# Performance work log

Hardware: AMD Instinct MI355X
Metric: run time of the kernel (lower is better)

## Reference

```python
import jax, jax.numpy as jnp
import numpy as np

B, T, C = 2, 2048, 1024
NH, NKV, HD = 16, 4, 64
VEC = 32  # ve_gate_channels


def _rope(x, cos, sin):
    d = x.shape[-1] // 2
    x1, x2 = x[..., :d], x[..., d:]
    return jnp.concatenate([x1 * cos + x2 * sin, -x1 * sin + x2 * cos], axis=-1)


def _rmsnorm(x):
    eps = jnp.finfo(x.dtype).eps
    return x * jax.lax.rsqrt(jnp.mean(x * x, axis=-1, keepdims=True) + eps)


def setup_inputs() -> dict:
    key = jax.random.key(0)
    ks = jax.random.split(key, 9)
    s = 0.02
    return {
        "x": jax.random.normal(ks[0], (B, T, C), jnp.float32),
        "ve": jax.random.normal(ks[1], (B, T, NKV * HD), jnp.float32),
        "cos": jax.random.normal(ks[2], (1, T, 1, HD // 2), jnp.float32),
        "sin": jax.random.normal(ks[3], (1, T, 1, HD // 2), jnp.float32),
        "Wq": jax.random.normal(ks[4], (C, NH * HD), jnp.float32) * s,
        "Wk": jax.random.normal(ks[5], (C, NKV * HD), jnp.float32) * s,
        "Wv": jax.random.normal(ks[6], (C, NKV * HD), jnp.float32) * s,
        "Wproj": jax.random.normal(ks[7], (C, C), jnp.float32) * s,
        "Wgate": jax.random.normal(ks[8], (VEC, NKV), jnp.float32) * s,
        "window_size": 1024,
    }


def reference(x, ve, cos, sin, Wq, Wk, Wv, Wproj, Wgate, window_size):
    Bx, Tx, Cx = x.shape
    q = (x @ Wq).reshape(Bx, Tx, NH, HD)
    k = (x @ Wk).reshape(Bx, Tx, NKV, HD)
    v = (x @ Wv).reshape(Bx, Tx, NKV, HD)

    # value-embedding gate (has_ve True for this layer)
    gate = 2.0 * jax.nn.sigmoid(x[..., :VEC] @ Wgate)  # [B,T,NKV]
    v = v + gate[..., None] * ve.reshape(Bx, Tx, NKV, HD)

    q, k = _rope(q, cos, sin), _rope(k, cos, sin)
    q, k = _rmsnorm(q), _rmsnorm(k)

    q = q.transpose(0, 2, 1, 3)  # [B,NH,T,HD]
    k = k.transpose(0, 2, 1, 3)  # [B,NKV,T,HD]
    v = v.transpose(0, 2, 1, 3)

    # GQA: each KV head serves NH//NKV consecutive q heads
    g = NH // NKV
    k = jnp.repeat(k, g, axis=1)
    v = jnp.repeat(v, g, axis=1)

    row = jnp.arange(Tx)[:, None]
    col = jnp.arange(Tx)[None, :]
    mask = (col <= row) & (col >= row - window_size)  # causal sliding window

    scores = jnp.einsum("bhqd,bhkd->bhqk", q, k) / np.sqrt(HD).astype(np.float32)
    scores = jnp.where(mask[None, None], scores, jnp.finfo(scores.dtype).min)
    attn = jax.nn.softmax(scores, axis=-1)
    y = jnp.einsum("bhqk,bhkd->bhqd", attn, v)

    y = y.transpose(0, 2, 1, 3).reshape(Bx, Tx, Cx)
    return y @ Wproj
```

## Files before the change

### kernel.cpp

```cpp
#include <hip/hip_runtime.h>

typedef __bf16 bf16x8 __attribute__((ext_vector_type(8)));
typedef __bf16 bf16x4 __attribute__((ext_vector_type(4)));
typedef float f32x4 __attribute__((ext_vector_type(4)));

__device__ inline float tof(float v) { return v; }
__device__ inline float tof(__bf16 v) { return (float)v; }

__device__ inline bf16x8 load8(const __bf16* p) { return *(const bf16x8*)p; }
__device__ inline bf16x8 load8(const float* p) {
    const float4 a = *(const float4*)p;
    const float4 b = *(const float4*)(p + 4);
    bf16x8 r;
    r[0] = (__bf16)a.x; r[1] = (__bf16)a.y; r[2] = (__bf16)a.z; r[3] = (__bf16)a.w;
    r[4] = (__bf16)b.x; r[5] = (__bf16)b.y; r[6] = (__bf16)b.z; r[7] = (__bf16)b.w;
    return r;
}

__device__ __forceinline__ void cp16(__bf16* lds, const __bf16* g) {
    __builtin_amdgcn_global_load_lds((__attribute__((address_space(1))) void*)g,
                                     (__attribute__((address_space(3))) void*)lds,
                                     16, 0, 0);
}

__global__ void sniff_kernel(const unsigned short* __restrict__ xs, int* flag) {
    int tid = threadIdx.x;
    int bad = 0;
    for (int i = tid; i < 512; i += 64) {
        unsigned int f = ((unsigned int)xs[i]) << 16;
        float v = __uint_as_float(f);
        float a = fabsf(v);
        if (!(a <= 1e4f) || (a != 0.f && a < 1e-6f)) bad++;
    }
    bad += __shfl_xor(bad, 1);  bad += __shfl_xor(bad, 2);
    bad += __shfl_xor(bad, 4);  bad += __shfl_xor(bad, 8);
    bad += __shfl_xor(bad, 16); bad += __shfl_xor(bad, 32);
    if (tid == 0) *flag = (bad > 32) ? 1 : 0;
}

template <typename T>
__device__ __forceinline__ void prep_body(
    const T* __restrict__ x, const T* __restrict__ ve,
    const T* __restrict__ cosp, const T* __restrict__ sinp,
    const T* __restrict__ Wq, const T* __restrict__ Wk,
    const T* __restrict__ Wv, const T* __restrict__ Wp, const T* __restrict__ Wg,
    __bf16* __restrict__ xb, __bf16* __restrict__ veb,
    float* __restrict__ cosf_, float* __restrict__ sinf_,
    __bf16* __restrict__ WqT, __bf16* __restrict__ WkT,
    __bf16* __restrict__ WvT, __bf16* __restrict__ WpT,
    float* __restrict__ gate, __bf16* tile)
{
    const int b = blockIdx.x, tid = threadIdx.x;

    if (b < 2624) {
        int g = b * 256 + tid;
        if (g < 524288) {
            *(bf16x8*)(xb + (size_t)g * 8) = load8(x + (size_t)g * 8);
        } else if (g < 655360) {
            int gg = g - 524288;
            *(bf16x8*)(veb + (size_t)gg * 8) = load8(ve + (size_t)gg * 8);
        } else if (g < 663552) {
            int gg = g - 655360;
            const T* s = cosp + (size_t)gg * 8; float* d = cosf_ + (size_t)gg * 8;
#pragma unroll
            for (int j = 0; j < 8; ++j) d[j] = tof(s[j]);
        } else {
            int gg = g - 663552;
            const T* s = sinp + (size_t)gg * 8; float* d = sinf_ + (size_t)gg * 8;
#pragma unroll
            for (int j = 0; j < 8; ++j) d[j] = tof(s[j]);
        }
    } else if (b < 3264) {
        int idx = b - 2624;
        const T* src; __bf16* dst; int C;
        if (idx < 256)      { src = Wq; dst = WqT; C = 1024; }
        else if (idx < 320) { src = Wk; dst = WkT; C = 256;  idx -= 256; }
        else if (idx < 384) { src = Wv; dst = WvT; C = 256;  idx -= 320; }
        else                { src = Wp; dst = WpT; C = 1024; idx -= 384; }
        const int ctiles = C >> 6;
        const int r0 = (idx / ctiles) * 64, c0 = (idx % ctiles) * 64;
#pragma unroll
        for (int i = 0; i < 2; ++i) {
            int c = tid + i * 256, ir = c >> 3, ic = (c & 7) * 8;
            *(bf16x8*)(&tile[ir * 72 + ic]) = load8(src + (size_t)(r0 + ir) * C + c0 + ic);
        }
        __syncthreads();
#pragma unroll
        for (int i = 0; i < 2; ++i) {
            int c = tid + i * 256, orr = c >> 3, okc = (c & 7) * 8;
            bf16x8 v;
#pragma unroll
            for (int j = 0; j < 8; ++j) v[j] = tile[(okc + j) * 72 + orr];
            *(bf16x8*)(dst + (size_t)(c0 + orr) * 1024 + r0 + okc) = v;
        }
    } else {
        int r = (b - 3264) * 256 + tid;
        float z[4] = {0.f, 0.f, 0.f, 0.f};
        for (int j = 0; j < 32; ++j) {
            float xv = tof(x[(size_t)r * 1024 + j]);
#pragma unroll
            for (int h = 0; h < 4; ++h) z[h] += xv * tof(Wg[j * 4 + h]);
        }
#pragma unroll
        for (int h = 0; h < 4; ++h) gate[r * 4 + h] = 2.f / (1.f + __expf(-z[h]));
    }
}

__global__ __launch_bounds__(256) void prep_kernel(
    const void* x, const void* ve, const void* cosp, const void* sinp,
    const void* Wq, const void* Wk, const void* Wv, const void* Wp, const void* Wg,
    __bf16* xb, __bf16* veb, float* cosf_, float* sinf_,
    __bf16* WqT, __bf16* WkT, __bf16* WvT, __bf16* WpT,
    float* gate, const int* __restrict__ flag)
{
    __shared__ __bf16 tile[64 * 72];
    if (*flag) {
        prep_body<float>((const float*)x, (const float*)ve, (const float*)cosp,
                         (const float*)sinp, (const float*)Wq, (const float*)Wk,
                         (const float*)Wv, (const float*)Wp, (const float*)Wg,
                         xb, veb, cosf_, sinf_, WqT, WkT, WvT, WpT, gate, tile);
    } else {
        prep_body<__bf16>((const __bf16*)x, (const __bf16*)ve, (const __bf16*)cosp,
                          (const __bf16*)sinp, (const __bf16*)Wq, (const __bf16*)Wk,
                          (const __bf16*)Wv, (const __bf16*)Wp, (const __bf16*)Wg,
                          xb, veb, cosf_, sinf_, WqT, WkT, WvT, WpT, gate, tile);
    }
}

__global__ __launch_bounds__(256) void qkv_kernel(
    const __bf16* __restrict__ xb,
    const __bf16* __restrict__ WqT, const __bf16* __restrict__ WkT,
    const __bf16* __restrict__ WvT, const __bf16* __restrict__ veb,
    const float* __restrict__ cosf_, const float* __restrict__ sinf_,
    const float* __restrict__ gate,
    __bf16* __restrict__ qo, __bf16* __restrict__ ko, __bf16* __restrict__ vTo)
{
    const int row0 = blockIdx.x * 128;
    const int cb = blockIdx.y;
    const __bf16* BT; int col0, h, mode;
    if (cb < 16)      { BT = WqT; col0 = cb * 64;        h = cb;      mode = 0; }
    else if (cb < 20) { BT = WkT; col0 = (cb - 16) * 64; h = cb - 16; mode = 1; }
    else              { BT = WvT; col0 = (cb - 20) * 64; h = cb - 20; mode = 2; }

    __shared__ __align__(16) __bf16 As[128 * 32];
    __shared__ __align__(16) __bf16 Bs[64 * 32];

    const int tid  = threadIdx.x;
    const int w    = tid >> 6;
    const int lane = tid & 63;
    const int quad = lane >> 4;
    const int l15  = lane & 15;
    const int wr   = w * 32;

    f32x4 acc[2][4];
#pragma unroll
    for (int mi = 0; mi < 2; ++mi)
#pragma unroll
        for (int nj = 0; nj < 4; ++nj) acc[mi][nj] = (f32x4){0.f, 0.f, 0.f, 0.f};

    for (int kk = 0; kk < 1024; kk += 32) {
#pragma unroll
        for (int i = 0; i < 2; ++i) {
            int c = i * 256 + (w << 6) + lane;
            int rr = c >> 2, kc = (c & 3) << 3;
            cp16(&As[c << 3], &xb[(size_t)(row0 + rr) * 1024 + kk + kc]);
        }
        {
            int c = (w << 6) + lane;
            int rr = c >> 2, kc = (c & 3) << 3;
            cp16(&Bs[c << 3], &BT[(size_t)(col0 + rr) * 1024 + kk + kc]);
        }
        __syncthreads();
        bf16x8 a[2], bfr[4];
#pragma unroll
        for (int mi = 0; mi < 2; ++mi) a[mi]  = *(const bf16x8*)(&As[(wr + mi * 16 + l15) * 32 + quad * 8]);
#pragma unroll
        for (int nj = 0; nj < 4; ++nj) bfr[nj] = *(const bf16x8*)(&Bs[(nj * 16 + l15) * 32 + quad * 8]);
#pragma unroll
        for (int mi = 0; mi < 2; ++mi)
#pragma unroll
            for (int nj = 0; nj < 4; ++nj)
                acc[mi][nj] = __builtin_amdgcn_mfma_f32_16x16x32_bf16(a[mi], bfr[nj], acc[mi][nj], 0, 0, 0);
        __syncthreads();
    }

    if (mode < 2) {
        __bf16* dst = (mode == 0) ? qo : ko;
        const int nh = (mode == 0) ? 16 : 4;
#pragma unroll
        for (int mi = 0; mi < 2; ++mi) {
#pragma unroll
            for (int r = 0; r < 4; ++r) {
                int row = row0 + wr + mi * 16 + quad * 4 + r;
                int b = row >> 11, t = row & 2047;
                float c0 = cosf_[t * 32 + l15];
                float c1 = cosf_[t * 32 + 16 + l15];
                float s0 = sinf_[t * 32 + l15];
                float s1 = sinf_[t * 32 + 16 + l15];
                float v0 =  c0 * acc[mi][0][r] + s0 * acc[mi][2][r];
                float v1 =  c1 * acc[mi][1][r] + s1 * acc[mi][3][r];
                float v2 = -s0 * acc[mi][0][r] + c0 * acc[mi][2][r];
                float v3 = -s1 * acc[mi][1][r] + c1 * acc[mi][3][r];
                float ss = v0 * v0 + v1 * v1 + v2 * v2 + v3 * v3;
                ss += __shfl_xor(ss, 1); ss += __shfl_xor(ss, 2);
                ss += __shfl_xor(ss, 4); ss += __shfl_xor(ss, 8);
                float sc = rsqrtf(ss * (1.f / 64.f) + 1.1920929e-7f);
                size_t base = (((size_t)b * nh + h) * 2048 + t) * 64;
                dst[base + 0 * 16 + l15] = (__bf16)(v0 * sc);
                dst[base + 1 * 16 + l15] = (__bf16)(v1 * sc);
                dst[base + 2 * 16 + l15] = (__bf16)(v2 * sc);
                dst[base + 3 * 16 + l15] = (__bf16)(v3 * sc);
            }
        }
    } else {
#pragma unroll
        for (int mi = 0; mi < 2; ++mi) {
            int rowb = row0 + wr + mi * 16 + quad * 4;
            int b = rowb >> 11, t0 = rowb & 2047;
#pragma unroll
            for (int nj = 0; nj < 4; ++nj) {
                int d = nj * 16 + l15;
                bf16x4 pack;
#pragma unroll
                for (int r = 0; r < 4; ++r) {
                    int row = rowb + r;
                    float g = gate[row * 4 + h];
                    float val = acc[mi][nj][r] + g * tof(veb[(size_t)row * 256 + h * 64 + d]);
                    pack[r] = (__bf16)val;
                }
                size_t a = (((size_t)b * 4 + h) * 64 + d) * 2048 + t0;
                *(bf16x4*)(&vTo[a]) = pack;
            }
        }
    }
}

__global__ __launch_bounds__(256) void attn_kernel(
    const __bf16* __restrict__ qg, const __bf16* __restrict__ kg,
    const __bf16* __restrict__ vTg, __bf16* __restrict__ yo,
    const int* __restrict__ winp)
{
    const int q0 = blockIdx.x * 128;
    const int hh = blockIdx.y, b = blockIdx.z;
    const int kvh = hh >> 2;
    const int W = winp[0];

    const int tid  = threadIdx.x;
    const int w    = tid >> 6;
    const int lane = tid & 63;
    const int quad = lane >> 4;
    const int l15  = lane & 15;

    __shared__ __align__(16) __bf16 Ks[2][64 * 64];
    __shared__ __align__(16) __bf16 Vt[2][64 * 64];
    __shared__ __align__(16) __bf16 Ps[4][32 * 72];

    bf16x8 qf[2][2];
#pragma unroll
    for (int i = 0; i < 2; ++i) {
        size_t qb = (((size_t)b * 16 + hh) * 2048 + q0 + w * 32 + i * 16 + l15) * 64;
        qf[i][0] = *(const bf16x8*)(&qg[qb + quad * 8]);
        qf[i][1] = *(const bf16x8*)(&qg[qb + 32 + quad * 8]);
    }

    f32x4 oacc[2][4];
    float lsum[2][4];
#pragma unroll
    for (int i = 0; i < 2; ++i)
#pragma unroll
        for (int n = 0; n < 4; ++n) {
            oacc[i][n] = (f32x4){0.f, 0.f, 0.f, 0.f};
            lsum[i][n] = 0.f;
        }

    const int lo = q0 - W;
    const int kt_lo = lo > 0 ? (lo >> 6) : 0;
    const int kt_hi = (q0 + 127) >> 6;
    const size_t kvbase = ((size_t)b * 4 + kvh) * 2048 * 64;

    auto stage = [&](int buf, int k0) {
#pragma unroll
        for (int i = 0; i < 2; ++i) {
            int c = i * 256 + tid;
            int rr = c >> 3;
            int jj = (c & 7) ^ (rr & 7);
            cp16(&Ks[buf][c * 8], &kg[kvbase + (size_t)(k0 + rr) * 64 + jj * 8]);
            cp16(&Vt[buf][c * 8], &vTg[kvbase + (size_t)rr * 2048 + k0 + jj * 8]);
        }
    };

    stage(0, kt_lo * 64);
    __syncthreads();

    int cur = 0;
    for (int kt = kt_lo; kt <= kt_hi; ++kt) {
        const int k0 = kt * 64;
        const bool need_mask = (k0 + 63 > q0) || (q0 + 127 - k0 > W);
        if (kt < kt_hi) stage(cur ^ 1, k0 + 64);

        f32x4 sacc[2][4];
#pragma unroll
        for (int i = 0; i < 2; ++i)
#pragma unroll
            for (int n = 0; n < 4; ++n) sacc[i][n] = (f32x4){0.f, 0.f, 0.f, 0.f};
        const __bf16* Kc = &Ks[cur][0];
#pragma unroll
        for (int n = 0; n < 4; ++n) {
            int m = n * 16 + l15;
            bf16x8 b0 = *(const bf16x8*)(&Kc[m * 64 + (quad ^ (m & 7)) * 8]);
            bf16x8 b1 = *(const bf16x8*)(&Kc[m * 64 + ((4 + quad) ^ (m & 7)) * 8]);
#pragma unroll
            for (int i = 0; i < 2; ++i) {
                sacc[i][n] = __builtin_amdgcn_mfma_f32_16x16x32_bf16(qf[i][0], b0, sacc[i][n], 0, 0, 0);
                sacc[i][n] = __builtin_amdgcn_mfma_f32_16x16x32_bf16(qf[i][1], b1, sacc[i][n], 0, 0, 0);
            }
        }

#pragma unroll
        for (int i = 0; i < 2; ++i) {
#pragma unroll
            for (int r = 0; r < 4; ++r) {
                const int row_g = q0 + w * 32 + i * 16 + quad * 4 + r;
#pragma unroll
                for (int n = 0; n < 4; ++n) {
                    float p = exp2f(fmaf(sacc[i][n][r], 0.18033688f, -11.5415603f));
                    if (need_mask) {
                        int col_g = k0 + n * 16 + l15;
                        bool ok = (col_g <= row_g) && (row_g - col_g <= W);
                        p = ok ? p : 0.f;
                    }
                    lsum[i][r] += p;
                    Ps[w][(i * 16 + quad * 4 + r) * 72 + n * 16 + l15] = (__bf16)p;
                }
            }
        }
        asm volatile("s_waitcnt lgkmcnt(0)" ::: "memory");

        const __bf16* Vc = &Vt[cur][0];
#pragma unroll
        for (int ks = 0; ks < 2; ++ks) {
            bf16x8 pfr0 = *(const bf16x8*)(&Ps[w][l15 * 72 + ks * 32 + quad * 8]);
            bf16x8 pfr1 = *(const bf16x8*)(&Ps[w][(16 + l15) * 72 + ks * 32 + quad * 8]);
#pragma unroll
            for (int n = 0; n < 4; ++n) {
                int m = n * 16 + l15;
                bf16x8 bv = *(const bf16x8*)(&Vc[m * 64 + ((ks * 4 + quad) ^ (m & 7)) * 8]);
                oacc[0][n] = __builtin_amdgcn_mfma_f32_16x16x32_bf16(pfr0, bv, oacc[0][n], 0, 0, 0);
                oacc[1][n] = __builtin_amdgcn_mfma_f32_16x16x32_bf16(pfr1, bv, oacc[1][n], 0, 0, 0);
            }
        }

        __syncthreads();
        cur ^= 1;
    }

#pragma unroll
    for (int i = 0; i < 2; ++i) {
#pragma unroll
        for (int r = 0; r < 4; ++r) {
            float l = lsum[i][r];
            l += __shfl_xor(l, 1); l += __shfl_xor(l, 2);
            l += __shfl_xor(l, 4); l += __shfl_xor(l, 8);
            float inv = 1.f / l;
            int t = q0 + w * 32 + i * 16 + quad * 4 + r;
            size_t base = ((size_t)(b * 2048 + t)) * 1024 + hh * 64;
#pragma unroll
            for (int n = 0; n < 4; ++n)
                yo[base + n * 16 + l15] = (__bf16)(oacc[i][n][r] * inv);
        }
    }
}

__global__ __launch_bounds__(256) void proj_kernel(
    const __bf16* __restrict__ y, const __bf16* __restrict__ WpT,
    void* __restrict__ outp, const int* __restrict__ flag)
{
    const int isf32 = *flag;
    const int row0 = blockIdx.x * 128;
    const int col0 = blockIdx.y * 64;
    __shared__ __align__(16) __bf16 As[128 * 32];
    __shared__ __align__(16) __bf16 Bs[64 * 32];

    const int tid  = threadIdx.x;
    const int w    = tid >> 6;
    const int lane = tid & 63;
    const int quad = lane >> 4;
    const int l15  = lane & 15;
    const int wr   = w * 32;

    f32x4 acc[2][4];
#pragma unroll
    for (int mi = 0; mi < 2; ++mi)
#pragma unroll
        for (int nj = 0; nj < 4; ++nj) acc[mi][nj] = (f32x4){0.f, 0.f, 0.f, 0.f};

    for (int kk = 0; kk < 1024; kk += 32) {
#pragma unroll
        for (int i = 0; i < 2; ++i) {
            int c = i * 256 + (w << 6) + lane;
            int rr = c >> 2, kc = (c & 3) << 3;
            cp16(&As[c << 3], &y[(size_t)(row0 + rr) * 1024 + kk + kc]);
        }
        {
            int c = (w << 6) + lane;
            int rr = c >> 2, kc = (c & 3) << 3;
            cp16(&Bs[c << 3], &WpT[(size_t)(col0 + rr) * 1024 + kk + kc]);
        }
        __syncthreads();
        bf16x8 a[2], bfr[4];
#pragma unroll
        for (int mi = 0; mi < 2; ++mi) a[mi]  = *(const bf16x8*)(&As[(wr + mi * 16 + l15) * 32 + quad * 8]);
#pragma unroll
        for (int nj = 0; nj < 4; ++nj) bfr[nj] = *(const bf16x8*)(&Bs[(nj * 16 + l15) * 32 + quad * 8]);
#pragma unroll
        for (int mi = 0; mi < 2; ++mi)
#pragma unroll
            for (int nj = 0; nj < 4; ++nj)
                acc[mi][nj] = __builtin_amdgcn_mfma_f32_16x16x32_bf16(a[mi], bfr[nj], acc[mi][nj], 0, 0, 0);
        __syncthreads();
    }

#pragma unroll
    for (int mi = 0; mi < 2; ++mi)
#pragma unroll
        for (int r = 0; r < 4; ++r) {
            int row = row0 + wr + mi * 16 + quad * 4 + r;
            if (isf32) {
                float* out = (float*)outp;
#pragma unroll
                for (int nj = 0; nj < 4; ++nj)
                    out[(size_t)row * 1024 + col0 + nj * 16 + l15] = acc[mi][nj][r];
            } else {
                __bf16* out = (__bf16*)outp;
#pragma unroll
                for (int nj = 0; nj < 4; ++nj)
                    out[(size_t)row * 1024 + col0 + nj * 16 + l15] = (__bf16)acc[mi][nj][r];
            }
        }
}

extern "C" void kernel_launch(void* const* d_in, const int* in_sizes, int n_in,
                              void* d_out, int out_size, void* d_ws, size_t ws_size,
                              hipStream_t stream) {
    const int* win = (const int*)d_in[9];

    char* p = (char*)d_ws;
    int*    flag = (int*)p;                    p += 256;
    __bf16* q_ws = (__bf16*)p;                 p += (size_t)4194304 * 2;
    __bf16* k_ws = (__bf16*)p;                 p += (size_t)1048576 * 2;
    __bf16* vT_ws= (__bf16*)p;                 p += (size_t)1048576 * 2;
    __bf16* y_ws = (__bf16*)p;                 p += (size_t)4194304 * 2;
    __bf16* xb   = (__bf16*)p;                 p += (size_t)4194304 * 2;
    __bf16* veb  = (__bf16*)p;                 p += (size_t)1048576 * 2;
    __bf16* WqT  = (__bf16*)p;                 p += (size_t)1048576 * 2;
    __bf16* WkT  = (__bf16*)p;                 p += (size_t)262144 * 2;
    __bf16* WvT  = (__bf16*)p;                 p += (size_t)262144 * 2;
    __bf16* WpT  = (__bf16*)p;                 p += (size_t)1048576 * 2;
    float*  cosf_ = (float*)p;                 p += (size_t)65536 * 4;
    float*  sinf_ = (float*)p;                 p += (size_t)65536 * 4;
    float*  gate  = (float*)p;                 p += (size_t)16384 * 4;

    sniff_kernel<<<1, 64, 0, stream>>>((const unsigned short*)d_in[0], flag);

    prep_kernel<<<3280, 256, 0, stream>>>(
        d_in[0], d_in[1], d_in[2], d_in[3], d_in[4], d_in[5], d_in[6], d_in[7],
        d_in[8], xb, veb, cosf_, sinf_, WqT, WkT, WvT, WpT, gate, flag);

    qkv_kernel<<<dim3(32, 24), 256, 0, stream>>>(xb, WqT, WkT, WvT, veb,
                                                 cosf_, sinf_, gate, q_ws, k_ws, vT_ws);

    attn_kernel<<<dim3(16, 16, 2), 256, 0, stream>>>(q_ws, k_ws, vT_ws, y_ws, win);

    proj_kernel<<<dim3(32, 16), 256, 0, stream>>>(y_ws, WpT, d_out, flag);
}
```

Before: 195.5 us.

## Fuse value-gate compute into QKV GEMM and halve attention query tile

```diff
diff --git a/kernel.cpp b/kernel.cpp
--- a/kernel.cpp
+++ b/kernel.cpp
@@ -48,11 +48,11 @@
     float* __restrict__ cosf_, float* __restrict__ sinf_,
     __bf16* __restrict__ WqT, __bf16* __restrict__ WkT,
     __bf16* __restrict__ WvT, __bf16* __restrict__ WpT,
-    float* __restrict__ gate, __bf16* tile)
+    __bf16* __restrict__ wgb, __bf16* tile)
 {
     const int b = blockIdx.x, tid = threadIdx.x;
 
-    if (b < 2624) {
+    if (b < 2625) {
         int g = b * 256 + tid;
         if (g < 524288) {
             *(bf16x8*)(xb + (size_t)g * 8) = load8(x + (size_t)g * 8);
@@ -64,14 +64,19 @@
             const T* s = cosp + (size_t)gg * 8; float* d = cosf_ + (size_t)gg * 8;
 #pragma unroll
             for (int j = 0; j < 8; ++j) d[j] = tof(s[j]);
-        } else {
+        } else if (g < 671744) {
             int gg = g - 663552;
             const T* s = sinp + (size_t)gg * 8; float* d = sinf_ + (size_t)gg * 8;
 #pragma unroll
             for (int j = 0; j < 8; ++j) d[j] = tof(s[j]);
-        }
-    } else if (b < 3264) {
-        int idx = b - 2624;
+        } else if (g < 671760) {
+            int gg = g - 671744;
+            const T* s = Wg + (size_t)gg * 8; __bf16* d = wgb + (size_t)gg * 8;
+#pragma unroll
+            for (int j = 0; j < 8; ++j) d[j] = (__bf16)tof(s[j]);
+        }
+    } else {
+        int idx = b - 2625;
         const T* src; __bf16* dst; int C;
         if (idx < 256)      { src = Wq; dst = WqT; C = 1024; }
         else if (idx < 320) { src = Wk; dst = WkT; C = 256;  idx -= 256; }
@@ -93,16 +98,6 @@
             for (int j = 0; j < 8; ++j) v[j] = tile[(okc + j) * 72 + orr];
             *(bf16x8*)(dst + (size_t)(c0 + orr) * 1024 + r0 + okc) = v;
         }
-    } else {
-        int r = (b - 3264) * 256 + tid;
-        float z[4] = {0.f, 0.f, 0.f, 0.f};
-        for (int j = 0; j < 32; ++j) {
-            float xv = tof(x[(size_t)r * 1024 + j]);
-#pragma unroll
-            for (int h = 0; h < 4; ++h) z[h] += xv * tof(Wg[j * 4 + h]);
-        }
-#pragma unroll
-        for (int h = 0; h < 4; ++h) gate[r * 4 + h] = 2.f / (1.f + __expf(-z[h]));
     }
 }
 
@@ -111,19 +106,19 @@
     const void* Wq, const void* Wk, const void* Wv, const void* Wp, const void* Wg,
     __bf16* xb, __bf16* veb, float* cosf_, float* sinf_,
     __bf16* WqT, __bf16* WkT, __bf16* WvT, __bf16* WpT,
-    float* gate, const int* __restrict__ flag)
+    __bf16* wgb, const int* __restrict__ flag)
 {
     __shared__ __bf16 tile[64 * 72];
     if (*flag) {
         prep_body<float>((const float*)x, (const float*)ve, (const float*)cosp,
                          (const float*)sinp, (const float*)Wq, (const float*)Wk,
                          (const float*)Wv, (const float*)Wp, (const float*)Wg,
-                         xb, veb, cosf_, sinf_, WqT, WkT, WvT, WpT, gate, tile);
+                         xb, veb, cosf_, sinf_, WqT, WkT, WvT, WpT, wgb, tile);
     } else {
         prep_body<__bf16>((const __bf16*)x, (const __bf16*)ve, (const __bf16*)cosp,
                           (const __bf16*)sinp, (const __bf16*)Wq, (const __bf16*)Wk,
                           (const __bf16*)Wv, (const __bf16*)Wp, (const __bf16*)Wg,
-                          xb, veb, cosf_, sinf_, WqT, WkT, WvT, WpT, gate, tile);
+                          xb, veb, cosf_, sinf_, WqT, WkT, WvT, WpT, wgb, tile);
     }
 }
 
@@ -132,7 +127,7 @@
     const __bf16* __restrict__ WqT, const __bf16* __restrict__ WkT,
     const __bf16* __restrict__ WvT, const __bf16* __restrict__ veb,
     const float* __restrict__ cosf_, const float* __restrict__ sinf_,
-    const float* __restrict__ gate,
+    const __bf16* __restrict__ wgb,
     __bf16* __restrict__ qo, __bf16* __restrict__ ko, __bf16* __restrict__ vTo)
 {
     const int row0 = blockIdx.x * 128;
@@ -158,6 +153,17 @@
 #pragma unroll
         for (int nj = 0; nj < 4; ++nj) acc[mi][nj] = (f32x4){0.f, 0.f, 0.f, 0.f};
 
+    bf16x8 wgB;
+#pragma unroll
+    for (int j = 0; j < 8; ++j) wgB[j] = (__bf16)0.f;
+    if (mode == 2 && l15 < 4) {
+#pragma unroll
+        for (int j = 0; j < 8; ++j) wgB[j] = wgb[(quad * 8 + j) * 4 + l15];
+    }
+    f32x4 zacc[2];
+    zacc[0] = (f32x4){0.f, 0.f, 0.f, 0.f};
+    zacc[1] = (f32x4){0.f, 0.f, 0.f, 0.f};
+
     for (int kk = 0; kk < 1024; kk += 32) {
 #pragma unroll
         for (int i = 0; i < 2; ++i) {
@@ -176,6 +182,10 @@
         for (int mi = 0; mi < 2; ++mi) a[mi]  = *(const bf16x8*)(&As[(wr + mi * 16 + l15) * 32 + quad * 8]);
 #pragma unroll
         for (int nj = 0; nj < 4; ++nj) bfr[nj] = *(const bf16x8*)(&Bs[(nj * 16 + l15) * 32 + quad * 8]);
+        if (mode == 2 && kk == 0) {
+            zacc[0] = __builtin_amdgcn_mfma_f32_16x16x32_bf16(a[0], wgB, zacc[0], 0, 0, 0);
+            zacc[1] = __builtin_amdgcn_mfma_f32_16x16x32_bf16(a[1], wgB, zacc[1], 0, 0, 0);
+        }
 #pragma unroll
         for (int mi = 0; mi < 2; ++mi)
 #pragma unroll
@@ -217,6 +227,12 @@
         for (int mi = 0; mi < 2; ++mi) {
             int rowb = row0 + wr + mi * 16 + quad * 4;
             int b = rowb >> 11, t0 = rowb & 2047;
+            float gg[4];
+#pragma unroll
+            for (int r = 0; r < 4; ++r) {
+                float zv = __shfl(zacc[mi][r], quad * 16 + h);
+                gg[r] = 2.f / (1.f + __expf(-zv));
+            }
 #pragma unroll
             for (int nj = 0; nj < 4; ++nj) {
                 int d = nj * 16 + l15;
@@ -224,8 +240,7 @@
 #pragma unroll
                 for (int r = 0; r < 4; ++r) {
                     int row = rowb + r;
-                    float g = gate[row * 4 + h];
-                    float val = acc[mi][nj][r] + g * tof(veb[(size_t)row * 256 + h * 64 + d]);
+                    float val = acc[mi][nj][r] + gg[r] * tof(veb[(size_t)row * 256 + h * 64 + d]);
                     pack[r] = (__bf16)val;
                 }
                 size_t a = (((size_t)b * 4 + h) * 64 + d) * 2048 + t0;
@@ -240,7 +255,7 @@
     const __bf16* __restrict__ vTg, __bf16* __restrict__ yo,
     const int* __restrict__ winp)
 {
-    const int q0 = blockIdx.x * 128;
+    const int q0 = blockIdx.x * 64;
     const int hh = blockIdx.y, b = blockIdx.z;
     const int kvh = hh >> 2;
     const int W = winp[0];
@@ -253,29 +268,20 @@
 
     __shared__ __align__(16) __bf16 Ks[2][64 * 64];
     __shared__ __align__(16) __bf16 Vt[2][64 * 64];
-    __shared__ __align__(16) __bf16 Ps[4][32 * 72];
-
-    bf16x8 qf[2][2];
-#pragma unroll
-    for (int i = 0; i < 2; ++i) {
-        size_t qb = (((size_t)b * 16 + hh) * 2048 + q0 + w * 32 + i * 16 + l15) * 64;
-        qf[i][0] = *(const bf16x8*)(&qg[qb + quad * 8]);
-        qf[i][1] = *(const bf16x8*)(&qg[qb + 32 + quad * 8]);
-    }
-
-    f32x4 oacc[2][4];
-    float lsum[2][4];
-#pragma unroll
-    for (int i = 0; i < 2; ++i)
-#pragma unroll
-        for (int n = 0; n < 4; ++n) {
-            oacc[i][n] = (f32x4){0.f, 0.f, 0.f, 0.f};
-            lsum[i][n] = 0.f;
-        }
+    __shared__ __align__(16) __bf16 Ps[4][16 * 72];
+
+    const size_t qb = (((size_t)b * 16 + hh) * 2048 + q0 + w * 16 + l15) * 64;
+    bf16x8 qf0 = *(const bf16x8*)(&qg[qb + quad * 8]);
+    bf16x8 qf1 = *(const bf16x8*)(&qg[qb + 32 + quad * 8]);
+
+    f32x4 oacc[4];
+    float lsum[4];
+#pragma unroll
+    for (int n = 0; n < 4; ++n) { oacc[n] = (f32x4){0.f, 0.f, 0.f, 0.f}; lsum[n] = 0.f; }
 
     const int lo = q0 - W;
     const int kt_lo = lo > 0 ? (lo >> 6) : 0;
-    const int kt_hi = (q0 + 127) >> 6;
+    const int kt_hi = q0 >> 6;
     const size_t kvbase = ((size_t)b * 4 + kvh) * 2048 * 64;
 
     auto stage = [&](int buf, int k0) {
@@ -295,43 +301,35 @@
     int cur = 0;
     for (int kt = kt_lo; kt <= kt_hi; ++kt) {
         const int k0 = kt * 64;
-        const bool need_mask = (k0 + 63 > q0) || (q0 + 127 - k0 > W);
+        const bool need_mask = (k0 + 63 > q0) || (q0 + 63 - k0 > W);
         if (kt < kt_hi) stage(cur ^ 1, k0 + 64);
 
-        f32x4 sacc[2][4];
-#pragma unroll
-        for (int i = 0; i < 2; ++i)
-#pragma unroll
-            for (int n = 0; n < 4; ++n) sacc[i][n] = (f32x4){0.f, 0.f, 0.f, 0.f};
+        f32x4 sacc[4];
+#pragma unroll
+        for (int n = 0; n < 4; ++n) sacc[n] = (f32x4){0.f, 0.f, 0.f, 0.f};
         const __bf16* Kc = &Ks[cur][0];
 #pragma unroll
         for (int n = 0; n < 4; ++n) {
             int m = n * 16 + l15;
             bf16x8 b0 = *(const bf16x8*)(&Kc[m * 64 + (quad ^ (m & 7)) * 8]);
             bf16x8 b1 = *(const bf16x8*)(&Kc[m * 64 + ((4 + quad) ^ (m & 7)) * 8]);
-#pragma unroll
-            for (int i = 0; i < 2; ++i) {
-                sacc[i][n] = __builtin_amdgcn_mfma_f32_16x16x32_bf16(qf[i][0], b0, sacc[i][n], 0, 0, 0);
-                sacc[i][n] = __builtin_amdgcn_mfma_f32_16x16x32_bf16(qf[i][1], b1, sacc[i][n], 0, 0, 0);
-            }
-        }
-
-#pragma unroll
-        for (int i = 0; i < 2; ++i) {
-#pragma unroll
-            for (int r = 0; r < 4; ++r) {
-                const int row_g = q0 + w * 32 + i * 16 + quad * 4 + r;
-#pragma unroll
-                for (int n = 0; n < 4; ++n) {
-                    float p = exp2f(fmaf(sacc[i][n][r], 0.18033688f, -11.5415603f));
-                    if (need_mask) {
-                        int col_g = k0 + n * 16 + l15;
-                        bool ok = (col_g <= row_g) && (row_g - col_g <= W);
-                        p = ok ? p : 0.f;
-                    }
-                    lsum[i][r] += p;
-                    Ps[w][(i * 16 + quad * 4 + r) * 72 + n * 16 + l15] = (__bf16)p;
+            sacc[n] = __builtin_amdgcn_mfma_f32_16x16x32_bf16(qf0, b0, sacc[n], 0, 0, 0);
+            sacc[n] = __builtin_amdgcn_mfma_f32_16x16x32_bf16(qf1, b1, sacc[n], 0, 0, 0);
+        }
+
+#pragma unroll
+        for (int r = 0; r < 4; ++r) {
+            const int row_g = q0 + w * 16 + quad * 4 + r;
+#pragma unroll
+            for (int n = 0; n < 4; ++n) {
+                float p = exp2f(fmaf(sacc[n][r], 0.18033688f, -11.5415603f));
+                if (need_mask) {
+                    int col_g = k0 + n * 16 + l15;
+                    bool ok = (col_g <= row_g) && (row_g - col_g <= W);
+                    p = ok ? p : 0.f;
                 }
+                lsum[r] += p;
+                Ps[w][(quad * 4 + r) * 72 + n * 16 + l15] = (__bf16)p;
             }
         }
         asm volatile("s_waitcnt lgkmcnt(0)" ::: "memory");
@@ -339,14 +337,12 @@
         const __bf16* Vc = &Vt[cur][0];
 #pragma unroll
         for (int ks = 0; ks < 2; ++ks) {
-            bf16x8 pfr0 = *(const bf16x8*)(&Ps[w][l15 * 72 + ks * 32 + quad * 8]);
-            bf16x8 pfr1 = *(const bf16x8*)(&Ps[w][(16 + l15) * 72 + ks * 32 + quad * 8]);
+            bf16x8 pfr = *(const bf16x8*)(&Ps[w][l15 * 72 + ks * 32 + quad * 8]);
 #pragma unroll
             for (int n = 0; n < 4; ++n) {
                 int m = n * 16 + l15;
                 bf16x8 bv = *(const bf16x8*)(&Vc[m * 64 + ((ks * 4 + quad) ^ (m & 7)) * 8]);
-                oacc[0][n] = __builtin_amdgcn_mfma_f32_16x16x32_bf16(pfr0, bv, oacc[0][n], 0, 0, 0);
-                oacc[1][n] = __builtin_amdgcn_mfma_f32_16x16x32_bf16(pfr1, bv, oacc[1][n], 0, 0, 0);
+                oacc[n] = __builtin_amdgcn_mfma_f32_16x16x32_bf16(pfr, bv, oacc[n], 0, 0, 0);
             }
         }
 
@@ -355,19 +351,16 @@
     }
 
 #pragma unroll
-    for (int i = 0; i < 2; ++i) {
-#pragma unroll
-        for (int r = 0; r < 4; ++r) {
-            float l = lsum[i][r];
-            l += __shfl_xor(l, 1); l += __shfl_xor(l, 2);
-            l += __shfl_xor(l, 4); l += __shfl_xor(l, 8);
-            float inv = 1.f / l;
-            int t = q0 + w * 32 + i * 16 + quad * 4 + r;
-            size_t base = ((size_t)(b * 2048 + t)) * 1024 + hh * 64;
-#pragma unroll
-            for (int n = 0; n < 4; ++n)
-                yo[base + n * 16 + l15] = (__bf16)(oacc[i][n][r] * inv);
-        }
+    for (int r = 0; r < 4; ++r) {
+        float l = lsum[r];
+        l += __shfl_xor(l, 1); l += __shfl_xor(l, 2);
+        l += __shfl_xor(l, 4); l += __shfl_xor(l, 8);
+        float inv = 1.f / l;
+        int t = q0 + w * 16 + quad * 4 + r;
+        size_t base = ((size_t)(b * 2048 + t)) * 1024 + hh * 64;
+#pragma unroll
+        for (int n = 0; n < 4; ++n)
+            yo[base + n * 16 + l15] = (__bf16)(oacc[n][r] * inv);
     }
 }
 
@@ -458,18 +451,18 @@
     __bf16* WpT  = (__bf16*)p;                 p += (size_t)1048576 * 2;
     float*  cosf_ = (float*)p;                 p += (size_t)65536 * 4;
     float*  sinf_ = (float*)p;                 p += (size_t)65536 * 4;
-    float*  gate  = (float*)p;                 p += (size_t)16384 * 4;
+    __bf16* wgb   = (__bf16*)p;                p += 256;
 
     sniff_kernel<<<1, 64, 0, stream>>>((const unsigned short*)d_in[0], flag);
 
-    prep_kernel<<<3280, 256, 0, stream>>>(
+    prep_kernel<<<3265, 256, 0, stream>>>(
         d_in[0], d_in[1], d_in[2], d_in[3], d_in[4], d_in[5], d_in[6], d_in[7],
-        d_in[8], xb, veb, cosf_, sinf_, WqT, WkT, WvT, WpT, gate, flag);
+        d_in[8], xb, veb, cosf_, sinf_, WqT, WkT, WvT, WpT, wgb, flag);
 
     qkv_kernel<<<dim3(32, 24), 256, 0, stream>>>(xb, WqT, WkT, WvT, veb,
-                                                 cosf_, sinf_, gate, q_ws, k_ws, vT_ws);
-
-    attn_kernel<<<dim3(16, 16, 2), 256, 0, stream>>>(q_ws, k_ws, vT_ws, y_ws, win);
+                                                 cosf_, sinf_, wgb, q_ws, k_ws, vT_ws);
+
+    attn_kernel<<<dim3(32, 16, 2), 256, 0, stream>>>(q_ws, k_ws, vT_ws, y_ws, win);
 
     proj_kernel<<<dim3(32, 16), 256, 0, stream>>>(y_ws, WpT, d_out, flag);
 }
```

Result: no change. 198.9 us (+1.7%).

## Enlarge QKV GEMM tile to 128x128 and fuse gate computation via MFMA

Applied to the files above, without the earlier changes.

```diff
diff --git a/kernel.cpp b/kernel.cpp
--- a/kernel.cpp
+++ b/kernel.cpp
@@ -48,11 +48,11 @@
     float* __restrict__ cosf_, float* __restrict__ sinf_,
     __bf16* __restrict__ WqT, __bf16* __restrict__ WkT,
     __bf16* __restrict__ WvT, __bf16* __restrict__ WpT,
-    float* __restrict__ gate, __bf16* tile)
+    __bf16* __restrict__ wgb, __bf16* tile)
 {
     const int b = blockIdx.x, tid = threadIdx.x;
 
-    if (b < 2624) {
+    if (b < 2625) {
         int g = b * 256 + tid;
         if (g < 524288) {
             *(bf16x8*)(xb + (size_t)g * 8) = load8(x + (size_t)g * 8);
@@ -64,14 +64,19 @@
             const T* s = cosp + (size_t)gg * 8; float* d = cosf_ + (size_t)gg * 8;
 #pragma unroll
             for (int j = 0; j < 8; ++j) d[j] = tof(s[j]);
-        } else {
+        } else if (g < 671744) {
             int gg = g - 663552;
             const T* s = sinp + (size_t)gg * 8; float* d = sinf_ + (size_t)gg * 8;
 #pragma unroll
             for (int j = 0; j < 8; ++j) d[j] = tof(s[j]);
-        }
-    } else if (b < 3264) {
-        int idx = b - 2624;
+        } else if (g < 671760) {
+            int gg = g - 671744;
+            const T* s = Wg + (size_t)gg * 8; __bf16* d = wgb + (size_t)gg * 8;
+#pragma unroll
+            for (int j = 0; j < 8; ++j) d[j] = (__bf16)tof(s[j]);
+        }
+    } else {
+        int idx = b - 2625;
         const T* src; __bf16* dst; int C;
         if (idx < 256)      { src = Wq; dst = WqT; C = 1024; }
         else if (idx < 320) { src = Wk; dst = WkT; C = 256;  idx -= 256; }
@@ -93,16 +98,6 @@
             for (int j = 0; j < 8; ++j) v[j] = tile[(okc + j) * 72 + orr];
             *(bf16x8*)(dst + (size_t)(c0 + orr) * 1024 + r0 + okc) = v;
         }
-    } else {
-        int r = (b - 3264) * 256 + tid;
-        float z[4] = {0.f, 0.f, 0.f, 0.f};
-        for (int j = 0; j < 32; ++j) {
-            float xv = tof(x[(size_t)r * 1024 + j]);
-#pragma unroll
-            for (int h = 0; h < 4; ++h) z[h] += xv * tof(Wg[j * 4 + h]);
-        }
-#pragma unroll
-        for (int h = 0; h < 4; ++h) gate[r * 4 + h] = 2.f / (1.f + __expf(-z[h]));
     }
 }
 
@@ -111,19 +106,19 @@
     const void* Wq, const void* Wk, const void* Wv, const void* Wp, const void* Wg,
     __bf16* xb, __bf16* veb, float* cosf_, float* sinf_,
     __bf16* WqT, __bf16* WkT, __bf16* WvT, __bf16* WpT,
-    float* gate, const int* __restrict__ flag)
+    __bf16* wgb, const int* __restrict__ flag)
 {
     __shared__ __bf16 tile[64 * 72];
     if (*flag) {
         prep_body<float>((const float*)x, (const float*)ve, (const float*)cosp,
                          (const float*)sinp, (const float*)Wq, (const float*)Wk,
                          (const float*)Wv, (const float*)Wp, (const float*)Wg,
-                         xb, veb, cosf_, sinf_, WqT, WkT, WvT, WpT, gate, tile);
+                         xb, veb, cosf_, sinf_, WqT, WkT, WvT, WpT, wgb, tile);
     } else {
         prep_body<__bf16>((const __bf16*)x, (const __bf16*)ve, (const __bf16*)cosp,
                           (const __bf16*)sinp, (const __bf16*)Wq, (const __bf16*)Wk,
                           (const __bf16*)Wv, (const __bf16*)Wp, (const __bf16*)Wg,
-                          xb, veb, cosf_, sinf_, WqT, WkT, WvT, WpT, gate, tile);
+                          xb, veb, cosf_, sinf_, WqT, WkT, WvT, WpT, wgb, tile);
     }
 }
 
@@ -132,31 +127,43 @@
     const __bf16* __restrict__ WqT, const __bf16* __restrict__ WkT,
     const __bf16* __restrict__ WvT, const __bf16* __restrict__ veb,
     const float* __restrict__ cosf_, const float* __restrict__ sinf_,
-    const float* __restrict__ gate,
+    const __bf16* __restrict__ wgb,
     __bf16* __restrict__ qo, __bf16* __restrict__ ko, __bf16* __restrict__ vTo)
 {
     const int row0 = blockIdx.x * 128;
     const int cb = blockIdx.y;
-    const __bf16* BT; int col0, h, mode;
-    if (cb < 16)      { BT = WqT; col0 = cb * 64;        h = cb;      mode = 0; }
-    else if (cb < 20) { BT = WkT; col0 = (cb - 16) * 64; h = cb - 16; mode = 1; }
-    else              { BT = WvT; col0 = (cb - 20) * 64; h = cb - 20; mode = 2; }
+    const __bf16* BT; int col0, mode;
+    if (cb < 8)       { BT = WqT; col0 = cb * 128;        mode = 0; }
+    else if (cb < 10) { BT = WkT; col0 = (cb - 8) * 128;  mode = 1; }
+    else              { BT = WvT; col0 = (cb - 10) * 128; mode = 2; }
 
     __shared__ __align__(16) __bf16 As[128 * 32];
-    __shared__ __align__(16) __bf16 Bs[64 * 32];
+    __shared__ __align__(16) __bf16 Bs[128 * 32];
 
     const int tid  = threadIdx.x;
     const int w    = tid >> 6;
     const int lane = tid & 63;
     const int quad = lane >> 4;
     const int l15  = lane & 15;
-    const int wr   = w * 32;
-
-    f32x4 acc[2][4];
-#pragma unroll
-    for (int mi = 0; mi < 2; ++mi)
+    const int wr   = (w >> 1) * 64, wc = (w & 1) * 64;
+    const int h    = (col0 + wc) >> 6;
+
+    f32x4 acc[4][4];
+#pragma unroll
+    for (int mi = 0; mi < 4; ++mi)
 #pragma unroll
         for (int nj = 0; nj < 4; ++nj) acc[mi][nj] = (f32x4){0.f, 0.f, 0.f, 0.f};
+
+    bf16x8 wgB;
+#pragma unroll
+    for (int j = 0; j < 8; ++j) wgB[j] = (__bf16)0.f;
+    if (mode == 2 && l15 < 4) {
+#pragma unroll
+        for (int j = 0; j < 8; ++j) wgB[j] = wgb[(quad * 8 + j) * 4 + l15];
+    }
+    f32x4 zacc[4];
+#pragma unroll
+    for (int mi = 0; mi < 4; ++mi) zacc[mi] = (f32x4){0.f, 0.f, 0.f, 0.f};
 
     for (int kk = 0; kk < 1024; kk += 32) {
 #pragma unroll
@@ -164,20 +171,21 @@
             int c = i * 256 + (w << 6) + lane;
             int rr = c >> 2, kc = (c & 3) << 3;
             cp16(&As[c << 3], &xb[(size_t)(row0 + rr) * 1024 + kk + kc]);
-        }
-        {
-            int c = (w << 6) + lane;
-            int rr = c >> 2, kc = (c & 3) << 3;
             cp16(&Bs[c << 3], &BT[(size_t)(col0 + rr) * 1024 + kk + kc]);
         }
         __syncthreads();
-        bf16x8 a[2], bfr[4];
-#pragma unroll
-        for (int mi = 0; mi < 2; ++mi) a[mi]  = *(const bf16x8*)(&As[(wr + mi * 16 + l15) * 32 + quad * 8]);
-#pragma unroll
-        for (int nj = 0; nj < 4; ++nj) bfr[nj] = *(const bf16x8*)(&Bs[(nj * 16 + l15) * 32 + quad * 8]);
-#pragma unroll
-        for (int mi = 0; mi < 2; ++mi)
+        bf16x8 a[4], bfr[4];
+#pragma unroll
+        for (int mi = 0; mi < 4; ++mi) a[mi]  = *(const bf16x8*)(&As[(wr + mi * 16 + l15) * 32 + quad * 8]);
+#pragma unroll
+        for (int nj = 0; nj < 4; ++nj) bfr[nj] = *(const bf16x8*)(&Bs[(wc + nj * 16 + l15) * 32 + quad * 8]);
+        if (mode == 2 && kk == 0) {
+#pragma unroll
+            for (int mi = 0; mi < 4; ++mi)
+                zacc[mi] = __builtin_amdgcn_mfma_f32_16x16x32_bf16(a[mi], wgB, zacc[mi], 0, 0, 0);
+        }
+#pragma unroll
+        for (int mi = 0; mi < 4; ++mi)
 #pragma unroll
             for (int nj = 0; nj < 4; ++nj)
                 acc[mi][nj] = __builtin_amdgcn_mfma_f32_16x16x32_bf16(a[mi], bfr[nj], acc[mi][nj], 0, 0, 0);
@@ -188,7 +196,7 @@
         __bf16* dst = (mode == 0) ? qo : ko;
         const int nh = (mode == 0) ? 16 : 4;
 #pragma unroll
-        for (int mi = 0; mi < 2; ++mi) {
+        for (int mi = 0; mi < 4; ++mi) {
 #pragma unroll
             for (int r = 0; r < 4; ++r) {
                 int row = row0 + wr + mi * 16 + quad * 4 + r;
@@ -214,9 +222,15 @@
         }
     } else {
 #pragma unroll
-        for (int mi = 0; mi < 2; ++mi) {
+        for (int mi = 0; mi < 4; ++mi) {
             int rowb = row0 + wr + mi * 16 + quad * 4;
             int b = rowb >> 11, t0 = rowb & 2047;
+            float gg[4];
+#pragma unroll
+            for (int r = 0; r < 4; ++r) {
+                float zv = __shfl(zacc[mi][r], quad * 16 + h);
+                gg[r] = 2.f / (1.f + __expf(-zv));
+            }
 #pragma unroll
             for (int nj = 0; nj < 4; ++nj) {
                 int d = nj * 16 + l15;
@@ -224,8 +238,7 @@
 #pragma unroll
                 for (int r = 0; r < 4; ++r) {
                     int row = rowb + r;
-                    float g = gate[row * 4 + h];
-                    float val = acc[mi][nj][r] + g * tof(veb[(size_t)row * 256 + h * 64 + d]);
+                    float val = acc[mi][nj][r] + gg[r] * tof(veb[(size_t)row * 256 + h * 64 + d]);
                     pack[r] = (__bf16)val;
                 }
                 size_t a = (((size_t)b * 4 + h) * 64 + d) * 2048 + t0;
@@ -458,16 +471,16 @@
     __bf16* WpT  = (__bf16*)p;                 p += (size_t)1048576 * 2;
     float*  cosf_ = (float*)p;                 p += (size_t)65536 * 4;
     float*  sinf_ = (float*)p;                 p += (size_t)65536 * 4;
-    float*  gate  = (float*)p;                 p += (size_t)16384 * 4;
+    __bf16* wgb   = (__bf16*)p;                p += 256;
 
     sniff_kernel<<<1, 64, 0, stream>>>((const unsigned short*)d_in[0], flag);
 
-    prep_kernel<<<3280, 256, 0, stream>>>(
+    prep_kernel<<<3265, 256, 0, stream>>>(
         d_in[0], d_in[1], d_in[2], d_in[3], d_in[4], d_in[5], d_in[6], d_in[7],
-        d_in[8], xb, veb, cosf_, sinf_, WqT, WkT, WvT, WpT, gate, flag);
-
-    qkv_kernel<<<dim3(32, 24), 256, 0, stream>>>(xb, WqT, WkT, WvT, veb,
-                                                 cosf_, sinf_, gate, q_ws, k_ws, vT_ws);
+        d_in[8], xb, veb, cosf_, sinf_, WqT, WkT, WvT, WpT, wgb, flag);
+
+    qkv_kernel<<<dim3(32, 12), 256, 0, stream>>>(xb, WqT, WkT, WvT, veb,
+                                                 cosf_, sinf_, wgb, q_ws, k_ws, vT_ws);
 
     attn_kernel<<<dim3(16, 16, 2), 256, 0, stream>>>(q_ws, k_ws, vT_ws, y_ws, win);
 
```

After: 198.6 us. Within noise of the previous version (+1.6%).
